# Kernel optimization log

Hardware: AMD Instinct MI355X
Metric: run time of the kernel (lower is better)

The kernel has to match this reference:

```python
import jax, jax.numpy as jnp
import numpy as np

N_HEAD = 16
N_KV = 4
N_EMBD = 2048
HEAD_DIM = N_EMBD // N_HEAD  # 128
GROUP = N_HEAD // N_KV       # 4 queries per kv head


def setup_inputs() -> dict:
    key = jax.random.key(0)
    ks = jax.random.split(key, 5)
    B, S = 2, 2048
    scale = 0.02
    return {
        "x": jax.random.normal(ks[0], (B, S, N_EMBD), dtype=jnp.float32),
        "Wq": jax.random.normal(ks[1], (N_EMBD, N_EMBD), dtype=jnp.float32) * scale,
        "Wk": jax.random.normal(ks[2], (N_EMBD, N_EMBD // GROUP), dtype=jnp.float32) * scale,
        "Wv": jax.random.normal(ks[3], (N_EMBD, N_EMBD // GROUP), dtype=jnp.float32) * scale,
        "Wo": jax.random.normal(ks[4], (N_EMBD, N_EMBD), dtype=jnp.float32) * scale,
    }


def reference(x, Wq, Wk, Wv, Wo):
    B, S, _ = x.shape
    scale = HEAD_DIM ** -0.5
    # projections (bias=False)
    q = (x @ Wq).reshape(B, S, N_KV, GROUP, HEAD_DIM)   # grouped query heads
    k = (x @ Wk).reshape(B, S, N_KV, HEAD_DIM)
    v = (x @ Wv).reshape(B, S, N_KV, HEAD_DIM)
    # scores: repeat_interleave of K over GROUP == broadcast over g axis
    scores = jnp.einsum('bqkgd,bskd->bkgqs', q, k) * scale  # [B,n_kv,g,S,S]
    causal = jnp.triu(jnp.ones((S, S), dtype=bool), k=1)
    scores = jnp.where(causal, jnp.finfo(scores.dtype).min, scores)
    attn = jax.nn.softmax(scores, axis=-1)
    out = jnp.einsum('bkgqs,bskd->bqkgd', attn, v)  # [B,S,n_kv,g,hd]
    out = out.reshape(B, S, N_EMBD)
    return out @ Wo
```

## Files before the change

kernel.cpp:

```cpp
#include <hip/hip_runtime.h>

typedef unsigned short u16;
typedef unsigned int u32;
typedef __attribute__((ext_vector_type(8))) __bf16 bh8;
typedef __attribute__((ext_vector_type(4))) float fx4;

#define AS1 __attribute__((address_space(1)))
#define AS3 __attribute__((address_space(3)))

__device__ __forceinline__ void gll16(const void* g, void* l) {
  void* gg = const_cast<void*>(g);
  __builtin_amdgcn_global_load_lds((AS1 void*)gg, (AS3 void*)l, 16, 0, 0);
}

__device__ __forceinline__ u16 f2b(float f) {
  union { float f; u32 u; } v; v.f = f;
  u32 r = v.u + 0x7FFFu + ((v.u >> 16) & 1u);
  return (u16)(r >> 16);
}

__device__ __forceinline__ fx4 fzero() { fx4 z = {0.f, 0.f, 0.f, 0.f}; return z; }

#define MFMA16(a, b, c) __builtin_amdgcn_mfma_f32_16x16x32_bf16(a, b, c, 0, 0, 0)

__global__ void k_cast(const float* __restrict__ in, u16* __restrict__ out, int n4) {
  int i = blockIdx.x * blockDim.x + threadIdx.x;
  if (i >= n4) return;
  float4 v = reinterpret_cast<const float4*>(in)[i];
  ushort4 o;
  o.x = f2b(v.x); o.y = f2b(v.y); o.z = f2b(v.z); o.w = f2b(v.w);
  reinterpret_cast<ushort4*>(out)[i] = o;
}

__global__ void k_transpose_cast(const float* __restrict__ in, u16* __restrict__ out,
                                 int R, int C) {
  __shared__ float t[32][33];
  int tx = threadIdx.x, ty = threadIdx.y;
  int r0 = blockIdx.y * 32, c0 = blockIdx.x * 32;
#pragma unroll
  for (int j = 0; j < 4; j++)
    t[ty + 8 * j][tx] = in[(size_t)(r0 + ty + 8 * j) * C + c0 + tx];
  __syncthreads();
#pragma unroll
  for (int j = 0; j < 4; j++)
    out[(size_t)(c0 + ty + 8 * j) * R + r0 + tx] = f2b(t[tx][ty + 8 * j]);
}

__global__ void k_transpose_v(const u16* __restrict__ in, u16* __restrict__ out) {
  __shared__ u16 t[32][33];
  int tx = threadIdx.x, ty = threadIdx.y;
  int s0 = blockIdx.x * 32, d0 = blockIdx.y * 32;
  int z = blockIdx.z, b = z >> 2, kv = z & 3;
#pragma unroll
  for (int j = 0; j < 4; j++)
    t[ty + 8 * j][tx] = in[(size_t)(b * 2048 + s0 + ty + 8 * j) * 512 + kv * 128 + d0 + tx];
  __syncthreads();
#pragma unroll
  for (int j = 0; j < 4; j++)
    out[(size_t)(z * 128 + d0 + ty + 8 * j) * 2048 + s0 + tx] = t[tx][ty + 8 * j];
}

__device__ __forceinline__ void gemm256(const u16* __restrict__ A, const u16* __restrict__ Bt,
                                        int bm, int bn, u16* Sm, fx4 (&acc)[8][4]) {
  u16* As = Sm;
  u16* Bs = Sm + 32768;
  const int tid = threadIdx.x;
  const int lane = tid & 63;
  const int i = lane & 15, g = lane >> 4;
  const int w = tid >> 6;
  const int wr = w >> 2, wc = w & 3;
  const int arow0 = wr * 128 + i;
  const int brow0 = wc * 64 + i;
  const int swz = i & 7;

  auto SHALF = [&](const u16* G, int grow0, u16* Ld, int kt) {
#pragma unroll
    for (int cc = 0; cc < 2; cc++) {
      int p = tid + cc * 512;
      int row = p >> 3;
      int lg = (p & 7) ^ (row & 7);
      gll16(G + (size_t)(grow0 + row) * 2048 + kt + lg * 8, Ld + p * 8);
    }
  };

  auto ITER = [&](const u16* cA, const u16* cB, u16* nA, u16* nB, int ktn, bool st) {
    bh8 bf[4][2];
#pragma unroll
    for (int nf = 0; nf < 4; nf++)
#pragma unroll
      for (int kk = 0; kk < 2; kk++)
        bf[nf][kk] = *reinterpret_cast<const bh8*>(
            cB + (brow0 + nf * 16) * 64 + (((kk * 4 + g) ^ swz) << 3));
#pragma unroll
    for (int mp = 0; mp < 4; mp++) {
      if (st && mp == 0) { SHALF(A, bm, nA, ktn); SHALF(Bt, bn, nB, ktn); }
      if (st && mp == 1) { SHALF(A, bm + 128, nA + 8192, ktn); SHALF(Bt, bn + 128, nB + 8192, ktn); }
      bh8 af[2][2];
#pragma unroll
      for (int mm = 0; mm < 2; mm++)
#pragma unroll
        for (int kk = 0; kk < 2; kk++)
          af[mm][kk] = *reinterpret_cast<const bh8*>(
              cA + (arow0 + (mp * 2 + mm) * 16) * 64 + (((kk * 4 + g) ^ swz) << 3));
      __builtin_amdgcn_s_setprio(1);
#pragma unroll
      for (int mm = 0; mm < 2; mm++)
#pragma unroll
        for (int nf = 0; nf < 4; nf++)
#pragma unroll
          for (int kk = 0; kk < 2; kk++)
            acc[mp * 2 + mm][nf] = MFMA16(af[mm][kk], bf[nf][kk], acc[mp * 2 + mm][nf]);
      __builtin_amdgcn_s_setprio(0);
    }
  };

  SHALF(A, bm, As, 0); SHALF(A, bm + 128, As + 8192, 0);
  SHALF(Bt, bn, Bs, 0); SHALF(Bt, bn + 128, Bs + 8192, 0);
  __syncthreads();
  for (int t = 0; t < 32; t += 2) {
    ITER(As, Bs, As + 16384, Bs + 16384, (t + 1) * 64, true);
    __syncthreads();
    ITER(As + 16384, Bs + 16384, As, Bs, (t + 2) * 64, t + 2 < 32);
    __syncthreads();
  }
}

__global__ __launch_bounds__(512, 2) void k_proj(const u16* __restrict__ xb,
                                                 const u16* __restrict__ Wt,
                                                 u16* __restrict__ Qb, u16* __restrict__ Kb,
                                                 u16* __restrict__ Vb) {
  __shared__ __align__(16) u16 Sm[65536];
  fx4 acc[8][4];
#pragma unroll
  for (int m = 0; m < 8; m++)
#pragma unroll
    for (int n = 0; n < 4; n++) acc[m][n] = fzero();
  const int bm = blockIdx.x * 256, by = blockIdx.y, bn = by * 256;
  gemm256(xb, Wt, bm, bn, Sm, acc);

  u16* Cp; int coff, ldc; float alpha;
  if (by < 8)       { Cp = Qb; coff = by * 256;        ldc = 2048; alpha = 0.08838834764831845f; }
  else if (by < 10) { Cp = Kb; coff = (by - 8) * 256;  ldc = 512;  alpha = 1.0f; }
  else              { Cp = Vb; coff = (by - 10) * 256; ldc = 512;  alpha = 1.0f; }

  const int lane = threadIdx.x & 63, w = threadIdx.x >> 6;
  const int wr = w >> 2, wc = w & 3, i = lane & 15, g = lane >> 4;
#pragma unroll
  for (int mf = 0; mf < 8; mf++)
#pragma unroll
    for (int nf = 0; nf < 4; nf++)
#pragma unroll
      for (int r = 0; r < 4; r++) {
        int row = bm + wr * 128 + mf * 16 + 4 * g + r;
        int col = coff + wc * 64 + nf * 16 + i;
        Cp[(size_t)row * ldc + col] = f2b(acc[mf][nf][r] * alpha);
      }
}

__global__ __launch_bounds__(512, 2) void k_gemm_out(const u16* __restrict__ Ob,
                                                     const u16* __restrict__ Wot,
                                                     float* __restrict__ C) {
  __shared__ __align__(16) u16 Sm[65536];
  fx4 acc[8][4];
#pragma unroll
  for (int m = 0; m < 8; m++)
#pragma unroll
    for (int n = 0; n < 4; n++) acc[m][n] = fzero();
  const int bm = blockIdx.x * 256, bn = blockIdx.y * 256;
  gemm256(Ob, Wot, bm, bn, Sm, acc);

  const int lane = threadIdx.x & 63, w = threadIdx.x >> 6;
  const int wr = w >> 2, wc = w & 3, i = lane & 15, g = lane >> 4;
#pragma unroll
  for (int mf = 0; mf < 8; mf++)
#pragma unroll
    for (int nf = 0; nf < 4; nf++)
#pragma unroll
      for (int r = 0; r < 4; r++) {
        int row = bm + wr * 128 + mf * 16 + 4 * g + r;
        int col = bn + wc * 64 + nf * 16 + i;
        C[(size_t)row * 2048 + col] = acc[mf][nf][r];
      }
}

__global__ __launch_bounds__(512, 4) void k_attn(const u16* __restrict__ Qb,
                                                 const u16* __restrict__ Kb,
                                                 const u16* __restrict__ Vt,
                                                 u16* __restrict__ Ob) {
  __shared__ __align__(16) u16 Ks0[64 * 128], Ks1[64 * 128];
  __shared__ __align__(16) u16 Vs0[128 * 64], Vs1[128 * 64];
  __shared__ __align__(16) u16 Pl[8][16 * 64];
  const int tid = threadIdx.x, lane = tid & 63, w = tid >> 6;
  const int i = lane & 15, g = lane >> 4;
  const int j = blockIdx.x;
  const int head = blockIdx.y, b = blockIdx.z, kv = head >> 2;
  const bool isA = (w >= 4);
  const int qt = isA ? j : (31 - j);
  const int qmin = qt * 64 + (w & 3) * 16;
  const int nt = 32 - j;
  const int myNt = isA ? (j + 1) : nt;

  const u16* Kbb = Kb + (size_t)b * 2048 * 512 + kv * 128;
  const u16* Vbb = Vt + (size_t)(b * 4 + kv) * 128 * 2048;

  bh8 qf[4];
  {
    const u16* qp = Qb + (size_t)(b * 2048 + qmin + i) * 2048 + head * 128 + g * 8;
#pragma unroll
    for (int kb = 0; kb < 4; kb++) qf[kb] = *reinterpret_cast<const bh8*>(qp + kb * 32);
  }

  fx4 o[8];
#pragma unroll
  for (int dt = 0; dt < 8; dt++) o[dt] = fzero();
  float m[4] = {-1e30f, -1e30f, -1e30f, -1e30f};
  float lp[4] = {0.f, 0.f, 0.f, 0.f};

  auto STAGE = [&](u16* Kd, u16* Vd, int s0) {
#pragma unroll
    for (int cc = 0; cc < 2; cc++) {
      int c = tid + cc * 512;
      gll16(Kbb + (size_t)(s0 + (c >> 4)) * 512 + (((c & 15) ^ ((c >> 4) & 7)) * 8),
            Kd + c * 8);
      gll16(Vbb + (size_t)(c >> 3) * 2048 + s0 + (((c & 7) ^ ((c >> 3) & 7)) * 8),
            Vd + c * 8);
    }
  };

  auto TILE = [&](const u16* Kbuf, const u16* Vbuf, int s0) {
    fx4 sc[4];
    __builtin_amdgcn_s_setprio(1);
#pragma unroll
    for (int st = 0; st < 4; st++) {
      sc[st] = fzero();
#pragma unroll
      for (int kb = 0; kb < 4; kb++) {
        bh8 kf = *reinterpret_cast<const bh8*>(Kbuf + (st * 16 + i) * 128 +
                                               (((kb * 4 + g) ^ (i & 7)) * 8));
        sc[st] = MFMA16(qf[kb], kf, sc[st]);
      }
    }
    __builtin_amdgcn_s_setprio(0);
    if (s0 + 63 > qmin) {
#pragma unroll
      for (int st = 0; st < 4; st++)
#pragma unroll
        for (int r = 0; r < 4; r++) {
          int s = s0 + st * 16 + i;
          int q = qmin + 4 * g + r;
          if (s > q) sc[st][r] = -1e30f;
        }
    }
    float pmax[4];
#pragma unroll
    for (int r = 0; r < 4; r++) {
      float v = fmaxf(fmaxf(sc[0][r], sc[1][r]), fmaxf(sc[2][r], sc[3][r]));
      v = fmaxf(v, __shfl_xor(v, 1));
      v = fmaxf(v, __shfl_xor(v, 2));
      v = fmaxf(v, __shfl_xor(v, 4));
      v = fmaxf(v, __shfl_xor(v, 8));
      pmax[r] = v;
    }
    int need = 0;
#pragma unroll
    for (int r = 0; r < 4; r++) need |= (pmax[r] > m[r] + 8.0f) ? 1 : 0;
    if (__any(need)) {
#pragma unroll
      for (int r = 0; r < 4; r++) {
        float mn = fmaxf(m[r], pmax[r]);
        float corr = __expf(m[r] - mn);
        m[r] = mn;
        lp[r] *= corr;
#pragma unroll
        for (int dt = 0; dt < 8; dt++) o[dt][r] *= corr;
      }
    }
    float p[4][4];
#pragma unroll
    for (int r = 0; r < 4; r++) {
#pragma unroll
      for (int st = 0; st < 4; st++) p[st][r] = __expf(sc[st][r] - m[r]);
      lp[r] += (p[0][r] + p[1][r]) + (p[2][r] + p[3][r]);
    }

#pragma unroll
    for (int st = 0; st < 4; st++)
#pragma unroll
      for (int r = 0; r < 4; r++) {
        int row = 4 * g + r;
        int cg = st * 2 + (i >> 3);
        Pl[w][row * 64 + ((cg ^ (row & 7)) << 3) + (i & 7)] = f2b(p[st][r]);
      }
    bh8 pf0 = *reinterpret_cast<const bh8*>(&Pl[w][i * 64 + ((g ^ (i & 7)) << 3)]);
    bh8 pf1 = *reinterpret_cast<const bh8*>(&Pl[w][i * 64 + (((4 + g) ^ (i & 7)) << 3)]);
    __builtin_amdgcn_s_setprio(1);
#pragma unroll
    for (int dt = 0; dt < 8; dt++) {
      bh8 v0 = *reinterpret_cast<const bh8*>(Vbuf + (dt * 16 + i) * 64 +
                                             ((g ^ (i & 7)) * 8));
      bh8 v1 = *reinterpret_cast<const bh8*>(Vbuf + (dt * 16 + i) * 64 +
                                             (((4 + g) ^ (i & 7)) * 8));
      o[dt] = MFMA16(pf0, v0, o[dt]);
      o[dt] = MFMA16(pf1, v1, o[dt]);
    }
    __builtin_amdgcn_s_setprio(0);
  };

  STAGE(Ks0, Vs0, 0);
  __syncthreads();
  for (int t = 0; t < nt; t += 2) {
    if (t + 1 < nt) STAGE(Ks1, Vs1, (t + 1) * 64);
    if (t < myNt) TILE(Ks0, Vs0, t * 64);
    __syncthreads();
    if (t + 1 >= nt) break;
    if (t + 2 < nt) STAGE(Ks0, Vs0, (t + 2) * 64);
    if (t + 1 < myNt) TILE(Ks1, Vs1, (t + 1) * 64);
    __syncthreads();
  }

#pragma unroll
  for (int r = 0; r < 4; r++) {
    float s = lp[r];
    s += __shfl_xor(s, 1);
    s += __shfl_xor(s, 2);
    s += __shfl_xor(s, 4);
    s += __shfl_xor(s, 8);
    float inv = 1.0f / s;
#pragma unroll
    for (int dt = 0; dt < 8; dt++)
      Ob[(size_t)(b * 2048 + qmin + 4 * g + r) * 2048 + head * 128 + dt * 16 + i] =
          f2b(o[dt][r] * inv);
  }
}

extern "C" void kernel_launch(void* const* d_in, const int* in_sizes, int n_in,
                              void* d_out, int out_size, void* d_ws, size_t ws_size,
                              hipStream_t stream) {
  (void)in_sizes; (void)n_in; (void)out_size; (void)ws_size;
  const float* x  = (const float*)d_in[0];
  const float* Wq = (const float*)d_in[1];
  const float* Wk = (const float*)d_in[2];
  const float* Wv = (const float*)d_in[3];
  const float* Wo = (const float*)d_in[4];

  char* ws = (char*)d_ws;
  size_t off = 0;
  auto alloc = [&](size_t bytes) {
    void* p = ws + off;
    off += (bytes + 255) & ~(size_t)255;
    return p;
  };
  u16* xb  = (u16*)alloc(8388608ull * 2);
  u16* Wqt = (u16*)alloc(4194304ull * 2);
  u16* Wkt = (u16*)alloc(1048576ull * 2);
  u16* Wvt = (u16*)alloc(1048576ull * 2);
  u16* Wot = (u16*)alloc(4194304ull * 2);
  u16* Qb  = (u16*)alloc(8388608ull * 2);
  u16* Kb  = (u16*)alloc(2097152ull * 2);
  u16* Vb  = (u16*)alloc(2097152ull * 2);
  u16* Vt  = (u16*)alloc(2097152ull * 2);
  u16* Ob  = xb;

  k_cast<<<8192, 256, 0, stream>>>(x, xb, 2097152);
  k_transpose_cast<<<dim3(64, 64), dim3(32, 8), 0, stream>>>(Wq, Wqt, 2048, 2048);
  k_transpose_cast<<<dim3(16, 64), dim3(32, 8), 0, stream>>>(Wk, Wkt, 2048, 512);
  k_transpose_cast<<<dim3(16, 64), dim3(32, 8), 0, stream>>>(Wv, Wvt, 2048, 512);
  k_transpose_cast<<<dim3(64, 64), dim3(32, 8), 0, stream>>>(Wo, Wot, 2048, 2048);
  k_proj<<<dim3(16, 12), 512, 0, stream>>>(xb, Wqt, Qb, Kb, Vb);
  k_transpose_v<<<dim3(64, 4, 8), dim3(32, 8), 0, stream>>>(Vb, Vt);
  k_attn<<<dim3(16, 16, 2), 512, 0, stream>>>(Qb, Kb, Vt, Ob);
  k_gemm_out<<<dim3(16, 8), 512, 0, stream>>>(Ob, Wot, (float*)d_out);
}
```

Measured before the change: 323.0 us.

## Interleave per-chunk global-to-LDS staging with MFMA phases using explicit waitcnt barriers

Reworks the double-buffered GEMM main loop in gemm256. The next K-tile is now loaded in four 64-row chunks, one issued per MFMA sub-phase, instead of two half-tile bursts. __syncthreads is replaced by raw s_barrier plus explicit s_waitcnt vmcnt, so a wave only waits for the older buffer's loads before reading LDS. The aim is to spread memory traffic across the compute phases and avoid full drains at each tile boundary. The cost is several extra barriers per iteration, and correctness now rests on the hand-counted vmcnt values.

```diff
diff --git a/kernel.cpp b/kernel.cpp
--- a/kernel.cpp
+++ b/kernel.cpp
@@ -22,6 +22,9 @@
 __device__ __forceinline__ fx4 fzero() { fx4 z = {0.f, 0.f, 0.f, 0.f}; return z; }
 
 #define MFMA16(a, b, c) __builtin_amdgcn_mfma_f32_16x16x32_bf16(a, b, c, 0, 0, 0)
+#define SBAR() asm volatile("s_barrier" ::: "memory")
+#define VMCNT2() asm volatile("s_waitcnt vmcnt(2)" ::: "memory")
+#define VMCNT0() asm volatile("s_waitcnt vmcnt(0)" ::: "memory")
 
 __global__ void k_cast(const float* __restrict__ in, u16* __restrict__ out, int n4) {
   int i = blockIdx.x * blockDim.x + threadIdx.x;
@@ -62,28 +65,30 @@
 
 __device__ __forceinline__ void gemm256(const u16* __restrict__ A, const u16* __restrict__ Bt,
                                         int bm, int bn, u16* Sm, fx4 (&acc)[8][4]) {
-  u16* As = Sm;
-  u16* Bs = Sm + 32768;
-  const int tid = threadIdx.x;
-  const int lane = tid & 63;
+  u16* As0 = Sm;          u16* As1 = Sm + 16384;
+  u16* Bs0 = Sm + 32768;  u16* Bs1 = Sm + 49152;
+  const int tid = threadIdx.x, lane = tid & 63;
   const int i = lane & 15, g = lane >> 4;
-  const int w = tid >> 6;
-  const int wr = w >> 2, wc = w & 3;
+  const int w = tid >> 6, wr = w >> 2, wc = w & 3;
   const int arow0 = wr * 128 + i;
   const int brow0 = wc * 64 + i;
   const int swz = i & 7;
-
-  auto SHALF = [&](const u16* G, int grow0, u16* Ld, int kt) {
-#pragma unroll
-    for (int cc = 0; cc < 2; cc++) {
-      int p = tid + cc * 512;
-      int row = p >> 3;
-      int lg = (p & 7) ^ (row & 7);
-      gll16(G + (size_t)(grow0 + row) * 2048 + kt + lg * 8, Ld + p * 8);
-    }
-  };
-
-  auto ITER = [&](const u16* cA, const u16* cB, u16* nA, u16* nB, int ktn, bool st) {
+  const int srow = tid >> 3;
+  const int lg = (tid & 7) ^ (srow & 7);
+  const size_t aoff = (size_t)(bm + srow) * 2048 + lg * 8;
+  const size_t boff = (size_t)(bn + srow) * 2048 + lg * 8;
+  const int dslot = tid * 8;
+
+  auto CHUNK = [&](int c, int ktn, u16* nA, u16* nB) {
+    gll16(A + aoff + (size_t)c * 64 * 2048 + ktn, nA + c * 4096 + dslot);
+    gll16(Bt + boff + (size_t)c * 64 * 2048 + ktn, nB + c * 4096 + dslot);
+  };
+
+  auto ITER = [&](const u16* cA, const u16* cB, u16* nA, u16* nB, int ktn, bool stage) {
+    if (stage) { CHUNK(0, ktn, nA, nB); VMCNT2(); }
+    else       { VMCNT0(); }
+    SBAR();
+    __builtin_amdgcn_sched_barrier(0);
     bh8 bf[4][2];
 #pragma unroll
     for (int nf = 0; nf < 4; nf++)
@@ -91,10 +96,27 @@
       for (int kk = 0; kk < 2; kk++)
         bf[nf][kk] = *reinterpret_cast<const bh8*>(
             cB + (brow0 + nf * 16) * 64 + (((kk * 4 + g) ^ swz) << 3));
-#pragma unroll
-    for (int mp = 0; mp < 4; mp++) {
-      if (st && mp == 0) { SHALF(A, bm, nA, ktn); SHALF(Bt, bn, nB, ktn); }
-      if (st && mp == 1) { SHALF(A, bm + 128, nA + 8192, ktn); SHALF(Bt, bn + 128, nB + 8192, ktn); }
+    {
+      bh8 af[2][2];
+#pragma unroll
+      for (int mm = 0; mm < 2; mm++)
+#pragma unroll
+        for (int kk = 0; kk < 2; kk++)
+          af[mm][kk] = *reinterpret_cast<const bh8*>(
+              cA + (arow0 + mm * 16) * 64 + (((kk * 4 + g) ^ swz) << 3));
+      __builtin_amdgcn_s_setprio(1);
+#pragma unroll
+      for (int mm = 0; mm < 2; mm++)
+#pragma unroll
+        for (int nf = 0; nf < 4; nf++)
+#pragma unroll
+          for (int kk = 0; kk < 2; kk++)
+            acc[mm][nf] = MFMA16(af[mm][kk], bf[nf][kk], acc[mm][nf]);
+      __builtin_amdgcn_s_setprio(0);
+    }
+    SBAR();
+#pragma unroll
+    for (int mp = 1; mp < 4; mp++) {
       bh8 af[2][2];
 #pragma unroll
       for (int mm = 0; mm < 2; mm++)
@@ -102,6 +124,8 @@
         for (int kk = 0; kk < 2; kk++)
           af[mm][kk] = *reinterpret_cast<const bh8*>(
               cA + (arow0 + (mp * 2 + mm) * 16) * 64 + (((kk * 4 + g) ^ swz) << 3));
+      if (stage) CHUNK(mp, ktn, nA, nB);
+      SBAR();
       __builtin_amdgcn_s_setprio(1);
 #pragma unroll
       for (int mm = 0; mm < 2; mm++)
@@ -111,17 +135,17 @@
           for (int kk = 0; kk < 2; kk++)
             acc[mp * 2 + mm][nf] = MFMA16(af[mm][kk], bf[nf][kk], acc[mp * 2 + mm][nf]);
       __builtin_amdgcn_s_setprio(0);
-    }
-  };
-
-  SHALF(A, bm, As, 0); SHALF(A, bm + 128, As + 8192, 0);
-  SHALF(Bt, bn, Bs, 0); SHALF(Bt, bn + 128, Bs + 8192, 0);
-  __syncthreads();
+      SBAR();
+    }
+  };
+
+#pragma unroll
+  for (int c = 0; c < 4; c++) CHUNK(c, 0, As0, Bs0);
+  VMCNT0();
+  SBAR();
   for (int t = 0; t < 32; t += 2) {
-    ITER(As, Bs, As + 16384, Bs + 16384, (t + 1) * 64, true);
-    __syncthreads();
-    ITER(As + 16384, Bs + 16384, As, Bs, (t + 2) * 64, t + 2 < 32);
-    __syncthreads();
+    ITER(As0, Bs0, As1, Bs1, (t + 1) * 64, true);
+    ITER(As1, Bs1, As0, Bs0, (t + 2) * 64, t + 2 < 32);
   }
 }
 
```

New measurement: 336.9 us. +4.3%, slower.

## Read V directly from global in attention and merge weight transposes

Applied to the files above, without the earlier changes.

The attention kernel no longer stages V tiles into LDS. Each lane instead loads its V fragments straight from the transposed V buffer in global memory, and launch bounds are raised to allow more resident blocks. The four weight transpose launches are merged into one kernel that dispatches on block index. This cuts LDS use and launch overhead, but V loads now go through global/L2 without coalesced LDS reuse across waves, which may add latency in the PV MFMA loop.

```diff
diff --git a/kernel.cpp b/kernel.cpp
--- a/kernel.cpp
+++ b/kernel.cpp
@@ -32,11 +32,20 @@
   reinterpret_cast<ushort4*>(out)[i] = o;
 }
 
-__global__ void k_transpose_cast(const float* __restrict__ in, u16* __restrict__ out,
-                                 int R, int C) {
+__global__ void k_transpose_all(const float* __restrict__ Wq, const float* __restrict__ Wk,
+                                const float* __restrict__ Wv, const float* __restrict__ Wo,
+                                u16* __restrict__ Wqt, u16* __restrict__ Wkt,
+                                u16* __restrict__ Wvt, u16* __restrict__ Wot) {
   __shared__ float t[32][33];
+  int id = blockIdx.x;
+  const float* in; u16* out; int C, bx, by;
+  if (id < 4096)      { in = Wq; out = Wqt; C = 2048; bx = id & 63; by = id >> 6; }
+  else if (id < 5120) { id -= 4096; in = Wk; out = Wkt; C = 512; bx = id & 15; by = id >> 4; }
+  else if (id < 6144) { id -= 5120; in = Wv; out = Wvt; C = 512; bx = id & 15; by = id >> 4; }
+  else                { id -= 6144; in = Wo; out = Wot; C = 2048; bx = id & 63; by = id >> 6; }
+  const int R = 2048;
   int tx = threadIdx.x, ty = threadIdx.y;
-  int r0 = blockIdx.y * 32, c0 = blockIdx.x * 32;
+  int r0 = by * 32, c0 = bx * 32;
 #pragma unroll
   for (int j = 0; j < 4; j++)
     t[ty + 8 * j][tx] = in[(size_t)(r0 + ty + 8 * j) * C + c0 + tx];
@@ -183,12 +192,11 @@
       }
 }
 
-__global__ __launch_bounds__(512, 4) void k_attn(const u16* __restrict__ Qb,
+__global__ __launch_bounds__(512, 6) void k_attn(const u16* __restrict__ Qb,
                                                  const u16* __restrict__ Kb,
                                                  const u16* __restrict__ Vt,
                                                  u16* __restrict__ Ob) {
   __shared__ __align__(16) u16 Ks0[64 * 128], Ks1[64 * 128];
-  __shared__ __align__(16) u16 Vs0[128 * 64], Vs1[128 * 64];
   __shared__ __align__(16) u16 Pl[8][16 * 64];
   const int tid = threadIdx.x, lane = tid & 63, w = tid >> 6;
   const int i = lane & 15, g = lane >> 4;
@@ -216,18 +224,16 @@
   float m[4] = {-1e30f, -1e30f, -1e30f, -1e30f};
   float lp[4] = {0.f, 0.f, 0.f, 0.f};
 
-  auto STAGE = [&](u16* Kd, u16* Vd, int s0) {
+  auto STAGE = [&](u16* Kd, int s0) {
 #pragma unroll
     for (int cc = 0; cc < 2; cc++) {
       int c = tid + cc * 512;
       gll16(Kbb + (size_t)(s0 + (c >> 4)) * 512 + (((c & 15) ^ ((c >> 4) & 7)) * 8),
             Kd + c * 8);
-      gll16(Vbb + (size_t)(c >> 3) * 2048 + s0 + (((c & 7) ^ ((c >> 3) & 7)) * 8),
-            Vd + c * 8);
-    }
-  };
-
-  auto TILE = [&](const u16* Kbuf, const u16* Vbuf, int s0) {
+    }
+  };
+
+  auto TILE = [&](const u16* Kbuf, int s0) {
     fx4 sc[4];
     __builtin_amdgcn_s_setprio(1);
 #pragma unroll
@@ -293,28 +299,27 @@
       }
     bh8 pf0 = *reinterpret_cast<const bh8*>(&Pl[w][i * 64 + ((g ^ (i & 7)) << 3)]);
     bh8 pf1 = *reinterpret_cast<const bh8*>(&Pl[w][i * 64 + (((4 + g) ^ (i & 7)) << 3)]);
+    const u16* vrow = Vbb + (size_t)i * 2048 + s0 + g * 8;
     __builtin_amdgcn_s_setprio(1);
 #pragma unroll
     for (int dt = 0; dt < 8; dt++) {
-      bh8 v0 = *reinterpret_cast<const bh8*>(Vbuf + (dt * 16 + i) * 64 +
-                                             ((g ^ (i & 7)) * 8));
-      bh8 v1 = *reinterpret_cast<const bh8*>(Vbuf + (dt * 16 + i) * 64 +
-                                             (((4 + g) ^ (i & 7)) * 8));
+      bh8 v0 = *reinterpret_cast<const bh8*>(vrow + (size_t)dt * 16 * 2048);
+      bh8 v1 = *reinterpret_cast<const bh8*>(vrow + (size_t)dt * 16 * 2048 + 32);
       o[dt] = MFMA16(pf0, v0, o[dt]);
       o[dt] = MFMA16(pf1, v1, o[dt]);
     }
     __builtin_amdgcn_s_setprio(0);
   };
 
-  STAGE(Ks0, Vs0, 0);
+  STAGE(Ks0, 0);
   __syncthreads();
   for (int t = 0; t < nt; t += 2) {
-    if (t + 1 < nt) STAGE(Ks1, Vs1, (t + 1) * 64);
-    if (t < myNt) TILE(Ks0, Vs0, t * 64);
+    if (t + 1 < nt) STAGE(Ks1, (t + 1) * 64);
+    if (t < myNt) TILE(Ks0, t * 64);
     __syncthreads();
     if (t + 1 >= nt) break;
-    if (t + 2 < nt) STAGE(Ks0, Vs0, (t + 2) * 64);
-    if (t + 1 < myNt) TILE(Ks1, Vs1, (t + 1) * 64);
+    if (t + 2 < nt) STAGE(Ks0, (t + 2) * 64);
+    if (t + 1 < myNt) TILE(Ks1, (t + 1) * 64);
     __syncthreads();
   }
 
@@ -362,10 +367,7 @@
   u16* Ob  = xb;
 
   k_cast<<<8192, 256, 0, stream>>>(x, xb, 2097152);
-  k_transpose_cast<<<dim3(64, 64), dim3(32, 8), 0, stream>>>(Wq, Wqt, 2048, 2048);
-  k_transpose_cast<<<dim3(16, 64), dim3(32, 8), 0, stream>>>(Wk, Wkt, 2048, 512);
-  k_transpose_cast<<<dim3(16, 64), dim3(32, 8), 0, stream>>>(Wv, Wvt, 2048, 512);
-  k_transpose_cast<<<dim3(64, 64), dim3(32, 8), 0, stream>>>(Wo, Wot, 2048, 2048);
+  k_transpose_all<<<10240, dim3(32, 8), 0, stream>>>(Wq, Wk, Wv, Wo, Wqt, Wkt, Wvt, Wot);
   k_proj<<<dim3(16, 12), 512, 0, stream>>>(xb, Wqt, Qb, Kb, Vb);
   k_transpose_v<<<dim3(64, 4, 8), dim3(32, 8), 0, stream>>>(Vb, Vt);
   k_attn<<<dim3(16, 16, 2), 512, 0, stream>>>(Qb, Kb, Vt, Ob);
```

Measured after the change: 549.1 us. 1.7x slower.

## Restructure GEMM main loop pipeline and merge weight transpose launches

Applied to the files above, without the earlier changes.

The shared GEMM loop is rewritten so each tile loads all A/B fragments into registers first, then issues a barrier and immediately starts global-to-LDS prefetch of the tile two steps ahead into the same buffer while MFMAs run. Partial vmcnt waits replace full __syncthreads, keeping one stage in flight. Separately, the four weight transpose-cast kernels are merged into one launch to cut launch overhead. Holding all A fragments in registers raises register pressure, and the hand-written waitcnt/barrier logic depends on exact load counts.

```diff
diff --git a/kernel.cpp b/kernel.cpp
--- a/kernel.cpp
+++ b/kernel.cpp
@@ -32,11 +32,20 @@
   reinterpret_cast<ushort4*>(out)[i] = o;
 }
 
-__global__ void k_transpose_cast(const float* __restrict__ in, u16* __restrict__ out,
-                                 int R, int C) {
+__global__ void k_transpose_all(const float* __restrict__ Wq, const float* __restrict__ Wk,
+                                const float* __restrict__ Wv, const float* __restrict__ Wo,
+                                u16* __restrict__ Wqt, u16* __restrict__ Wkt,
+                                u16* __restrict__ Wvt, u16* __restrict__ Wot) {
   __shared__ float t[32][33];
+  int id = blockIdx.x;
+  const float* in; u16* out; int C, bx, by;
+  if (id < 4096)      { in = Wq; out = Wqt; C = 2048; bx = id & 63; by = id >> 6; }
+  else if (id < 5120) { id -= 4096; in = Wk; out = Wkt; C = 512; bx = id & 15; by = id >> 4; }
+  else if (id < 6144) { id -= 5120; in = Wv; out = Wvt; C = 512; bx = id & 15; by = id >> 4; }
+  else                { id -= 6144; in = Wo; out = Wot; C = 2048; bx = id & 63; by = id >> 6; }
+  const int R = 2048;
   int tx = threadIdx.x, ty = threadIdx.y;
-  int r0 = blockIdx.y * 32, c0 = blockIdx.x * 32;
+  int r0 = by * 32, c0 = bx * 32;
 #pragma unroll
   for (int j = 0; j < 4; j++)
     t[ty + 8 * j][tx] = in[(size_t)(r0 + ty + 8 * j) * C + c0 + tx];
@@ -62,29 +71,30 @@
 
 __device__ __forceinline__ void gemm256(const u16* __restrict__ A, const u16* __restrict__ Bt,
                                         int bm, int bn, u16* Sm, fx4 (&acc)[8][4]) {
-  u16* As = Sm;
-  u16* Bs = Sm + 32768;
-  const int tid = threadIdx.x;
-  const int lane = tid & 63;
+  u16* As0 = Sm;          u16* As1 = Sm + 16384;
+  u16* Bs0 = Sm + 32768;  u16* Bs1 = Sm + 49152;
+  const int tid = threadIdx.x, lane = tid & 63;
   const int i = lane & 15, g = lane >> 4;
-  const int w = tid >> 6;
-  const int wr = w >> 2, wc = w & 3;
+  const int w = tid >> 6, wr = w >> 2, wc = w & 3;
   const int arow0 = wr * 128 + i;
   const int brow0 = wc * 64 + i;
   const int swz = i & 7;
-
-  auto SHALF = [&](const u16* G, int grow0, u16* Ld, int kt) {
-#pragma unroll
-    for (int cc = 0; cc < 2; cc++) {
-      int p = tid + cc * 512;
-      int row = p >> 3;
-      int lg = (p & 7) ^ (row & 7);
-      gll16(G + (size_t)(grow0 + row) * 2048 + kt + lg * 8, Ld + p * 8);
-    }
-  };
-
-  auto ITER = [&](const u16* cA, const u16* cB, u16* nA, u16* nB, int ktn, bool st) {
-    bh8 bf[4][2];
+  const int srow = tid >> 3;
+  const int lg = (tid & 7) ^ (srow & 7);
+  const size_t aoff = (size_t)(bm + srow) * 2048 + lg * 8;
+  const size_t boff = (size_t)(bn + srow) * 2048 + lg * 8;
+  const int dslot = tid * 8;
+
+  auto STAGE = [&](int kt, u16* dA, u16* dB) {
+#pragma unroll
+    for (int c = 0; c < 4; c++) {
+      gll16(A + aoff + (size_t)c * 64 * 2048 + kt, dA + c * 4096 + dslot);
+      gll16(Bt + boff + (size_t)c * 64 * 2048 + kt, dB + c * 4096 + dslot);
+    }
+  };
+
+  auto TILE = [&](u16* cA, u16* cB, int ktn, bool st, bool last) {
+    bh8 bf[4][2], af[8][2];
 #pragma unroll
     for (int nf = 0; nf < 4; nf++)
 #pragma unroll
@@ -92,36 +102,36 @@
         bf[nf][kk] = *reinterpret_cast<const bh8*>(
             cB + (brow0 + nf * 16) * 64 + (((kk * 4 + g) ^ swz) << 3));
 #pragma unroll
-    for (int mp = 0; mp < 4; mp++) {
-      if (st && mp == 0) { SHALF(A, bm, nA, ktn); SHALF(Bt, bn, nB, ktn); }
-      if (st && mp == 1) { SHALF(A, bm + 128, nA + 8192, ktn); SHALF(Bt, bn + 128, nB + 8192, ktn); }
-      bh8 af[2][2];
-#pragma unroll
-      for (int mm = 0; mm < 2; mm++)
+    for (int mf = 0; mf < 8; mf++)
+#pragma unroll
+      for (int kk = 0; kk < 2; kk++)
+        af[mf][kk] = *reinterpret_cast<const bh8*>(
+            cA + (arow0 + mf * 16) * 64 + (((kk * 4 + g) ^ swz) << 3));
+    asm volatile("s_waitcnt lgkmcnt(0)" ::: "memory");
+    __builtin_amdgcn_sched_barrier(0);
+    asm volatile("s_barrier" ::: "memory");
+    if (st) STAGE(ktn, cA, cB);
+    __builtin_amdgcn_s_setprio(1);
+#pragma unroll
+    for (int mf = 0; mf < 8; mf++)
+#pragma unroll
+      for (int nf = 0; nf < 4; nf++)
 #pragma unroll
         for (int kk = 0; kk < 2; kk++)
-          af[mm][kk] = *reinterpret_cast<const bh8*>(
-              cA + (arow0 + (mp * 2 + mm) * 16) * 64 + (((kk * 4 + g) ^ swz) << 3));
-      __builtin_amdgcn_s_setprio(1);
-#pragma unroll
-      for (int mm = 0; mm < 2; mm++)
-#pragma unroll
-        for (int nf = 0; nf < 4; nf++)
-#pragma unroll
-          for (int kk = 0; kk < 2; kk++)
-            acc[mp * 2 + mm][nf] = MFMA16(af[mm][kk], bf[nf][kk], acc[mp * 2 + mm][nf]);
-      __builtin_amdgcn_s_setprio(0);
-    }
-  };
-
-  SHALF(A, bm, As, 0); SHALF(A, bm + 128, As + 8192, 0);
-  SHALF(Bt, bn, Bs, 0); SHALF(Bt, bn + 128, Bs + 8192, 0);
-  __syncthreads();
+          acc[mf][nf] = MFMA16(af[mf][kk], bf[nf][kk], acc[mf][nf]);
+    __builtin_amdgcn_s_setprio(0);
+    if (last) asm volatile("s_waitcnt vmcnt(0)" ::: "memory");
+    else      asm volatile("s_waitcnt vmcnt(8)" ::: "memory");
+    asm volatile("s_barrier" ::: "memory");
+  };
+
+  STAGE(0, As0, Bs0);
+  STAGE(64, As1, Bs1);
+  asm volatile("s_waitcnt vmcnt(8)" ::: "memory");
+  asm volatile("s_barrier" ::: "memory");
   for (int t = 0; t < 32; t += 2) {
-    ITER(As, Bs, As + 16384, Bs + 16384, (t + 1) * 64, true);
-    __syncthreads();
-    ITER(As + 16384, Bs + 16384, As, Bs, (t + 2) * 64, t + 2 < 32);
-    __syncthreads();
+    TILE(As0, Bs0, (t + 2) * 64, t + 2 < 32, t + 2 >= 32);
+    TILE(As1, Bs1, (t + 3) * 64, t + 3 < 32, t + 3 >= 32);
   }
 }
 
@@ -362,10 +372,7 @@
   u16* Ob  = xb;
 
   k_cast<<<8192, 256, 0, stream>>>(x, xb, 2097152);
-  k_transpose_cast<<<dim3(64, 64), dim3(32, 8), 0, stream>>>(Wq, Wqt, 2048, 2048);
-  k_transpose_cast<<<dim3(16, 64), dim3(32, 8), 0, stream>>>(Wk, Wkt, 2048, 512);
-  k_transpose_cast<<<dim3(16, 64), dim3(32, 8), 0, stream>>>(Wv, Wvt, 2048, 512);
-  k_transpose_cast<<<dim3(64, 64), dim3(32, 8), 0, stream>>>(Wo, Wot, 2048, 2048);
+  k_transpose_all<<<10240, dim3(32, 8), 0, stream>>>(Wq, Wk, Wv, Wo, Wqt, Wkt, Wvt, Wot);
   k_proj<<<dim3(16, 12), 512, 0, stream>>>(xb, Wqt, Qb, Kb, Vb);
   k_transpose_v<<<dim3(64, 4, 8), dim3(32, 8), 0, stream>>>(Vb, Vt);
   k_attn<<<dim3(16, 16, 2), 512, 0, stream>>>(Qb, Kb, Vt, Ob);
```

New measurement: 419.8 us. 30.0% more time.
